# Optimization experiments

Hardware: AMD Instinct MI355X
Metric: run time of the kernel (lower is better)

The kernel has to match this reference:

```python
import jax, jax.numpy as jnp
import numpy as np

LL = 1 << 20            # Fastfood padded size (power of 2 >= DD)
DD = 1024 * 768         # out_features * in_features
OUT, IN = 1024, 768


def fwht(v):
    """Unnormalized fast Walsh-Hadamard transform over a length-2^k vector."""
    n = v.shape[0]
    h = 1
    while h < n:
        v = v.reshape(-1, 2, h)
        v = jnp.concatenate([v[:, 0] + v[:, 1], v[:, 0] - v[:, 1]], axis=-1)
        h *= 2
    return v.reshape(n)


def setup_inputs() -> dict:
    key = jax.random.key(0)
    ks = jax.random.split(key, 7)
    x = jax.random.normal(ks[0], (8, 2048, IN), dtype=jnp.float32)
    theta = jax.random.normal(ks[1], (2048,), dtype=jnp.float32)
    W_0 = jax.random.normal(ks[2], (OUT, IN), dtype=jnp.float32) * 0.02
    b = jax.random.normal(ks[3], (OUT,), dtype=jnp.float32) * 0.02
    # Rademacher +/-1 diagonal
    BB = (jax.random.bernoulli(ks[4], 0.5, (LL,)).astype(jnp.float32) * 2.0 - 1.0)
    GG = jax.random.normal(ks[5], (LL,), dtype=jnp.float32)
    Pi = jax.random.permutation(ks[6], LL).astype(jnp.int64)
    return {"x": x, "theta": theta, "W_0": W_0, "b": b, "BB": BB, "GG": GG, "Pi": Pi}


def reference(x, theta, W_0, b, BB, GG, Pi):
    # pad intrinsic parameter to LL (theta.numel() < LL branch)
    theta_pad = jnp.zeros((LL,), dtype=theta.dtype).at[: theta.shape[0]].set(theta)
    # Fastfood: H B theta -> permute -> G diag -> H
    v = fwht(BB * theta_pad)
    v = v[Pi] * GG
    v = fwht(v)
    divisor = jnp.sqrt(LL * jnp.sum(GG * GG))
    update_vec = v[:DD] / (divisor * np.sqrt(float(DD) / LL))
    W_eff = W_0 + update_vec.reshape(OUT, IN)
    return jnp.einsum("bsi,oi->bso", x, W_eff) + b
```

## Files before the change

kernel.cpp:

```cpp
#include <hip/hip_runtime.h>
#include <hip/hip_bf16.h>


#define LL (1 << 20)
#define DD (1024 * 768)
#define OUTF 1024
#define INF 768
#define MROWS 16384

typedef __attribute__((ext_vector_type(8))) short s16x8;
typedef __attribute__((ext_vector_type(4))) float f32x4;
typedef __attribute__((ext_vector_type(16))) float f32x16;

__device__ __forceinline__ unsigned short f2bf(float f) {
    union { float f; unsigned u; } v; v.f = f;
    unsigned r = v.u + 0x7FFF + ((v.u >> 16) & 1);
    return (unsigned short)(r >> 16);
}

__device__ __forceinline__ unsigned cvt_pk_bf16(float lo, float hi) {
    unsigned r;
    asm("v_cvt_pk_bf16_f32 %0, %1, %2" : "=v"(r) : "v"(lo), "v"(hi));
    return r;
}

__global__ void k0_r01(const float* __restrict__ BB, const float* __restrict__ theta,
                       float* __restrict__ r01g) {
    __shared__ float sx[2048];
    const int t = threadIdx.x;
    const int r = t >> 7, tt = t & 127, lane = t & 63;
    float v[8];
    {
        const float4 a0 = *(const float4*)&BB[r * 1024 + tt * 8];
        const float4 a1 = *(const float4*)&BB[r * 1024 + tt * 8 + 4];
        const float4 b0 = *(const float4*)&theta[r * 1024 + tt * 8];
        const float4 b1 = *(const float4*)&theta[r * 1024 + tt * 8 + 4];
        v[0] = a0.x * b0.x; v[1] = a0.y * b0.y; v[2] = a0.z * b0.z; v[3] = a0.w * b0.w;
        v[4] = a1.x * b1.x; v[5] = a1.y * b1.y; v[6] = a1.z * b1.z; v[7] = a1.w * b1.w;
    }
    float a;
    a = v[0]; v[0] = a + v[1]; v[1] = a - v[1];
    a = v[2]; v[2] = a + v[3]; v[3] = a - v[3];
    a = v[4]; v[4] = a + v[5]; v[5] = a - v[5];
    a = v[6]; v[6] = a + v[7]; v[7] = a - v[7];
    a = v[0]; v[0] = a + v[2]; v[2] = a - v[2];
    a = v[1]; v[1] = a + v[3]; v[3] = a - v[3];
    a = v[4]; v[4] = a + v[6]; v[6] = a - v[6];
    a = v[5]; v[5] = a + v[7]; v[7] = a - v[7];
    a = v[0]; v[0] = a + v[4]; v[4] = a - v[4];
    a = v[1]; v[1] = a + v[5]; v[5] = a - v[5];
    a = v[2]; v[2] = a + v[6]; v[6] = a - v[6];
    a = v[3]; v[3] = a + v[7]; v[7] = a - v[7];
    #pragma unroll
    for (int j = 0; j < 6; j++) {
        const float sgn = ((lane >> j) & 1) ? -1.0f : 1.0f;
        #pragma unroll
        for (int c = 0; c < 8; c++) {
            float o = __shfl_xor(v[c], 1 << j, 64);
            v[c] = fmaf(sgn, v[c], o);
        }
    }
    #pragma unroll
    for (int c = 0; c < 8; c++) sx[r * 1024 + tt * 8 + c] = v[c];
    __syncthreads();
    {
        const int pt = r * 1024 + (tt ^ 64) * 8;
        const float sgn = (tt & 64) ? -1.0f : 1.0f;
        #pragma unroll
        for (int c = 0; c < 8; c++) v[c] = fmaf(sgn, v[c], sx[pt + c]);
    }
    #pragma unroll
    for (int c = 0; c < 8; c++) r01g[r * 1024 + tt * 8 + c] = v[c];
}

__global__ void k1_cast(const float* __restrict__ X, ushort* __restrict__ XB) {
    const f32x4* X4 = (const f32x4*)X;
    s16x8* O = (s16x8*)XB;
    size_t i = (size_t)blockIdx.x * 256 + threadIdx.x;
    #pragma unroll
    for (int j = 0; j < 3; j++, i += 524288) {
        const f32x4 A = X4[2 * i];
        const f32x4 B = X4[2 * i + 1];
        union { s16x8 v; unsigned u[4]; } o;
        o.u[0] = cvt_pk_bf16(A.x, A.y);
        o.u[1] = cvt_pk_bf16(A.z, A.w);
        o.u[2] = cvt_pk_bf16(B.x, B.y);
        o.u[3] = cvt_pk_bf16(B.z, B.w);
        O[i] = o.v;
    }
}

__global__ __launch_bounds__(1024)
void k3_gather_fwht_lo(const int* __restrict__ Pi, const float* __restrict__ GG,
                       const float* __restrict__ r01g, f32x4* __restrict__ T2,
                       float* __restrict__ partial) {
    __shared__ float r01s[2048];
    __shared__ f32x4 sA[1024];
    __shared__ float sB[4 * 1028];
    __shared__ float ws[16];
    const int t = threadIdx.x;
    const int s_r = t >> 8, tt = t & 255, lane = t & 63;
    const int row = blockIdx.x * 4 + s_r;

    r01s[t] = r01g[t];
    r01s[t + 1024] = r01g[t + 1024];
    const int4   pv = ((const int4*)Pi)[row * 256 + tt];
    const float4 gv = ((const float4*)GG)[row * 256 + tt];
    float g2 = gv.x * gv.x + gv.y * gv.y + gv.z * gv.z + gv.w * gv.w;
    #pragma unroll
    for (int o = 32; o > 0; o >>= 1) g2 += __shfl_down(g2, o, 64);
    if (lane == 0) ws[t >> 6] = g2;
    __syncthreads();

    float v[4];
    {
        int p; float g;
        p = pv.x; g = gv.x;
        v[0] = (r01s[p & 1023] + (((p >> 10) & 1) ? -1.0f : 1.0f) * r01s[1024 + (p & 1023)]) * g;
        p = pv.y; g = gv.y;
        v[1] = (r01s[p & 1023] + (((p >> 10) & 1) ? -1.0f : 1.0f) * r01s[1024 + (p & 1023)]) * g;
        p = pv.z; g = gv.z;
        v[2] = (r01s[p & 1023] + (((p >> 10) & 1) ? -1.0f : 1.0f) * r01s[1024 + (p & 1023)]) * g;
        p = pv.w; g = gv.w;
        v[3] = (r01s[p & 1023] + (((p >> 10) & 1) ? -1.0f : 1.0f) * r01s[1024 + (p & 1023)]) * g;
    }
    float a;
    a = v[0]; v[0] = a + v[1]; v[1] = a - v[1];
    a = v[2]; v[2] = a + v[3]; v[3] = a - v[3];
    a = v[0]; v[0] = a + v[2]; v[2] = a - v[2];
    a = v[1]; v[1] = a + v[3]; v[3] = a - v[3];
    #pragma unroll
    for (int j = 0; j < 6; j++) {
        const float sgn = ((lane >> j) & 1) ? -1.0f : 1.0f;
        #pragma unroll
        for (int c = 0; c < 4; c++) {
            float o = __shfl_xor(v[c], 1 << j, 64);
            v[c] = fmaf(sgn, v[c], o);
        }
    }
    {
        f32x4 vv; vv.x = v[0]; vv.y = v[1]; vv.z = v[2]; vv.w = v[3];
        sA[t] = vv;
    }
    __syncthreads();
    {
        const int b = t & ~192;
        const f32x4 q00 = sA[b];
        const f32x4 q10 = sA[b + 64];
        const f32x4 q01 = sA[b + 128];
        const f32x4 q11 = sA[b + 192];
        const float s8 = (tt & 64) ? -1.0f : 1.0f;
        const float s9 = (tt & 128) ? -1.0f : 1.0f;
        #pragma unroll
        for (int c = 0; c < 4; c++)
            v[c] = (q00[c] + s9 * q01[c]) + s8 * (q10[c] + s9 * q11[c]);
    }
    if (t == 0) {
        float s = 0;
        #pragma unroll
        for (int i = 0; i < 16; i++) s += ws[i];
        partial[blockIdx.x] = s;
    }
    {
        f32x4 vv; vv.x = v[0]; vv.y = v[1]; vv.z = v[2]; vv.w = v[3];
        *(f32x4*)&sB[s_r * 1028 + 4 * tt] = vv;
    }
    __syncthreads();
    {
        const int rl = t & 3;
        const int lo4 = t >> 2;
        const f32x4 w = *(const f32x4*)&sB[rl * 1028 + lo4 * 4];
        T2[(size_t)lo4 * 1024 + blockIdx.x * 4 + rl] = w;
    }
}

__global__ __launch_bounds__(1024)
void k4_fwht_hi(const f32x4* __restrict__ T2, const float* __restrict__ partial,
                const float* __restrict__ W0, ushort* __restrict__ WB) {
    __shared__ f32x4 sx[1024];
    __shared__ float rw[17];
    const int t = threadIdx.x;
    const int g = blockIdx.x;
    const int lane = t & 63;

    float pr = 0.0f;
    if (t < 256) pr = partial[t];
    #pragma unroll
    for (int o = 32; o > 0; o >>= 1) pr += __shfl_down(pr, o, 64);
    if (t < 256 && lane == 0) rw[t >> 6] = pr;

    f32x4 vv = T2[(size_t)g * 1024 + t];
    #pragma unroll
    for (int j = 0; j < 6; j++) {
        const float sgn = ((lane >> j) & 1) ? -1.0f : 1.0f;
        #pragma unroll
        for (int c = 0; c < 4; c++) {
            float o = __shfl_xor(vv[c], 1 << j, 64);
            vv[c] = fmaf(sgn, vv[c], o);
        }
    }
    sx[t] = vv;
    __syncthreads();
    if (t == 0) rw[16] = rw[0] + rw[1] + rw[2] + rw[3];
    {
        const int b = t & ~192;
        const f32x4 q00 = sx[b];
        const f32x4 q10 = sx[b + 64];
        const f32x4 q01 = sx[b + 128];
        const f32x4 q11 = sx[b + 192];
        const float s6 = (t & 64) ? -1.0f : 1.0f;
        const float s7 = (t & 128) ? -1.0f : 1.0f;
        #pragma unroll
        for (int c = 0; c < 4; c++)
            vv[c] = (q00[c] + s7 * q01[c]) + s6 * (q10[c] + s7 * q11[c]);
    }
    __syncthreads();
    sx[t] = vv;
    __syncthreads();
    {
        const int b = t & ~768;
        const f32x4 q00 = sx[b];
        const f32x4 q10 = sx[b + 256];
        const f32x4 q01 = sx[b + 512];
        const f32x4 q11 = sx[b + 768];
        const float s8 = (t & 256) ? -1.0f : 1.0f;
        const float s9 = (t & 512) ? -1.0f : 1.0f;
        #pragma unroll
        for (int c = 0; c < 4; c++)
            vv[c] = (q00[c] + s9 * q01[c]) + s8 * (q10[c] + s9 * q11[c]);
    }
    if (t < 768) {
        const float scale = rsqrtf(rw[16] * (float)DD);
        const size_t d = (size_t)t * 1024 + 4 * g;
        const float4 w = *(const float4*)&W0[d];
        ushort4 o;
        o.x = f2bf(w.x + vv.x * scale);
        o.y = f2bf(w.y + vv.y * scale);
        o.z = f2bf(w.z + vv.z * scale);
        o.w = f2bf(w.w + vv.w * scale);
        *(ushort4*)&WB[d] = o;
    }
}

#define BM 128
#define BN 128
#define BK 64

__global__ __launch_bounds__(256)
void k7_gemm(const ushort* __restrict__ A, const ushort* __restrict__ B,
             const float* __restrict__ bias, float* __restrict__ C) {
    __shared__ ushort As[BM * BK];
    __shared__ ushort Bs[BN * BK];
    const int tid  = threadIdx.x;
    const int lane = tid & 63;
    const int wave = tid >> 6;
    const int m0 = blockIdx.x * BM;
    const int n0 = blockIdx.y * BN;
    const int wm = (wave & 1) * 64;
    const int wn = (wave >> 1) * 64;

    const int fr_row = lane & 31;
    const int fr_kh  = lane >> 5;

    f32x16 acc[2][2];
    #pragma unroll
    for (int i = 0; i < 2; i++)
        #pragma unroll
        for (int j = 0; j < 2; j++) acc[i][j] = (f32x16)(0.0f);

    for (int kt = 0; kt < INF; kt += BK) {
        #pragma unroll
        for (int i = 0; i < 4; i++) {
            const int s   = i * 256 + tid;
            const int row = s >> 3;
            const int kc  = (s & 7) ^ (row & 7);
            const ushort* ga = A + (size_t)(m0 + row) * INF + kt + kc * 8;
            const ushort* gb = B + (size_t)(n0 + row) * INF + kt + kc * 8;
            __builtin_amdgcn_global_load_lds(
                (const __attribute__((address_space(1))) void*)ga,
                (__attribute__((address_space(3))) void*)&As[i * 2048 + wave * 512], 16, 0, 0);
            __builtin_amdgcn_global_load_lds(
                (const __attribute__((address_space(1))) void*)gb,
                (__attribute__((address_space(3))) void*)&Bs[i * 2048 + wave * 512], 16, 0, 0);
        }
        __syncthreads();

        #pragma unroll
        for (int ks = 0; ks < 4; ks++) {
            const int kc = ks * 2 + fr_kh;
            s16x8 af[2], bf[2];
            #pragma unroll
            for (int mi = 0; mi < 2; mi++) {
                const int r = wm + mi * 32 + fr_row;
                af[mi] = *(const s16x8*)&As[(r * 8 + (kc ^ (r & 7))) * 8];
            }
            #pragma unroll
            for (int ni = 0; ni < 2; ni++) {
                const int r = wn + ni * 32 + fr_row;
                bf[ni] = *(const s16x8*)&Bs[(r * 8 + (kc ^ (r & 7))) * 8];
            }
            #pragma unroll
            for (int mi = 0; mi < 2; mi++)
                #pragma unroll
                for (int ni = 0; ni < 2; ni++)
                    acc[mi][ni] = __builtin_amdgcn_mfma_f32_32x32x16_bf16(
                        af[mi], bf[ni], acc[mi][ni], 0, 0, 0);
        }
        __syncthreads();
    }

    const int ccol = lane & 31;
    const int rbase = (lane >> 5) * 4;
    #pragma unroll
    for (int ni = 0; ni < 2; ni++) {
        const int n = n0 + wn + ni * 32 + ccol;
        const float bv = bias[n];
        #pragma unroll
        for (int mi = 0; mi < 2; mi++) {
            const int mb = m0 + wm + mi * 32 + rbase;
            #pragma unroll
            for (int r = 0; r < 16; r++) {
                const int m = mb + (r & 3) + 8 * (r >> 2);
                C[(size_t)m * OUTF + n] = acc[mi][ni][r] + bv;
            }
        }
    }
}

extern "C" void kernel_launch(void* const* d_in, const int* in_sizes, int n_in,
                              void* d_out, int out_size, void* d_ws, size_t ws_size,
                              hipStream_t stream) {
    (void)in_sizes; (void)n_in; (void)out_size; (void)ws_size;
    const float* x     = (const float*)d_in[0];
    const float* theta = (const float*)d_in[1];
    const float* W0    = (const float*)d_in[2];
    const float* bias  = (const float*)d_in[3];
    const float* BB    = (const float*)d_in[4];
    const float* GG    = (const float*)d_in[5];
    const int*   Pi    = (const int*)d_in[6];
    float* out = (float*)d_out;

    char* ws = (char*)d_ws;
    ushort* XB   = (ushort*)ws;
    f32x4*  T2   = (f32x4*)(ws + 25165824);
    ushort* WB   = (ushort*)(ws + 29360128);
    float*  R01  = (float*)(ws + 30932992);
    float*  PART = (float*)(ws + 30941184);

    k0_r01          <<<1,    256, 0, stream>>>(BB, theta, R01);
    k1_cast         <<<2048, 256, 0, stream>>>(x, XB);
    k3_gather_fwht_lo<<<256, 1024, 0, stream>>>(Pi, GG, R01, T2, PART);
    k4_fwht_hi      <<<256, 1024, 0, stream>>>(T2, PART, W0, WB);
    k7_gemm<<<dim3(MROWS/BM, OUTF/BN), 256, 0, stream>>>(XB, WB, bias, out);
}
```

Measured before the change: 170.9 us.

## Double-buffer GEMM LDS tiles and merge cast with r01 kernel

The GEMM now keeps two LDS buffers, so the global-to-LDS loads for the next K tile are issued before the MFMA work on the current tile, with the aim of overlapping memory latency with compute. The one-block r01 kernel is also folded into the x-to-bf16 cast kernel as an extra block, removing one launch. Double buffering doubles LDS use per block to 64KB, which may lower occupancy. The loop also has to keep a barrier between compute and the next overwrite of the buffer, which cannot be confirmed from the visible lines.

```diff
diff --git a/kernel.cpp b/kernel.cpp
--- a/kernel.cpp
+++ b/kernel.cpp
@@ -24,10 +24,28 @@
     return r;
 }
 
-__global__ void k0_r01(const float* __restrict__ BB, const float* __restrict__ theta,
-                       float* __restrict__ r01g) {
+__global__ void k01_cast_r01(const float* __restrict__ X, ushort* __restrict__ XB,
+                             const float* __restrict__ BB, const float* __restrict__ theta,
+                             float* __restrict__ r01g) {
     __shared__ float sx[2048];
     const int t = threadIdx.x;
+    if (blockIdx.x < 2048) {
+        const f32x4* X4 = (const f32x4*)X;
+        s16x8* O = (s16x8*)XB;
+        size_t i = (size_t)blockIdx.x * 256 + t;
+        #pragma unroll
+        for (int j = 0; j < 3; j++, i += 524288) {
+            const f32x4 A = X4[2 * i];
+            const f32x4 B = X4[2 * i + 1];
+            union { s16x8 v; unsigned u[4]; } o;
+            o.u[0] = cvt_pk_bf16(A.x, A.y);
+            o.u[1] = cvt_pk_bf16(A.z, A.w);
+            o.u[2] = cvt_pk_bf16(B.x, B.y);
+            o.u[3] = cvt_pk_bf16(B.z, B.w);
+            O[i] = o.v;
+        }
+        return;
+    }
     const int r = t >> 7, tt = t & 127, lane = t & 63;
     float v[8];
     {
@@ -73,23 +91,6 @@
     for (int c = 0; c < 8; c++) r01g[r * 1024 + tt * 8 + c] = v[c];
 }
 
-__global__ void k1_cast(const float* __restrict__ X, ushort* __restrict__ XB) {
-    const f32x4* X4 = (const f32x4*)X;
-    s16x8* O = (s16x8*)XB;
-    size_t i = (size_t)blockIdx.x * 256 + threadIdx.x;
-    #pragma unroll
-    for (int j = 0; j < 3; j++, i += 524288) {
-        const f32x4 A = X4[2 * i];
-        const f32x4 B = X4[2 * i + 1];
-        union { s16x8 v; unsigned u[4]; } o;
-        o.u[0] = cvt_pk_bf16(A.x, A.y);
-        o.u[1] = cvt_pk_bf16(A.z, A.w);
-        o.u[2] = cvt_pk_bf16(B.x, B.y);
-        o.u[3] = cvt_pk_bf16(B.z, B.w);
-        O[i] = o.v;
-    }
-}
-
 __global__ __launch_bounds__(1024)
 void k3_gather_fwht_lo(const int* __restrict__ Pi, const float* __restrict__ GG,
                        const float* __restrict__ r01g, f32x4* __restrict__ T2,
@@ -245,12 +246,13 @@
 #define BM 128
 #define BN 128
 #define BK 64
+#define KITERS (INF / BK)
 
 __global__ __launch_bounds__(256)
 void k7_gemm(const ushort* __restrict__ A, const ushort* __restrict__ B,
              const float* __restrict__ bias, float* __restrict__ C) {
-    __shared__ ushort As[BM * BK];
-    __shared__ ushort Bs[BN * BK];
+    __shared__ ushort As[2][BM * BK];
+    __shared__ ushort Bs[2][BN * BK];
     const int tid  = threadIdx.x;
     const int lane = tid & 63;
     const int wave = tid >> 6;
@@ -268,7 +270,7 @@
         #pragma unroll
         for (int j = 0; j < 2; j++) acc[i][j] = (f32x16)(0.0f);
 
-    for (int kt = 0; kt < INF; kt += BK) {
+    auto stage = [&](int bsel, int kt) {
         #pragma unroll
         for (int i = 0; i < 4; i++) {
             const int s   = i * 256 + tid;
@@ -278,13 +280,22 @@
             const ushort* gb = B + (size_t)(n0 + row) * INF + kt + kc * 8;
             __builtin_amdgcn_global_load_lds(
                 (const __attribute__((address_space(1))) void*)ga,
-                (__attribute__((address_space(3))) void*)&As[i * 2048 + wave * 512], 16, 0, 0);
+                (__attribute__((address_space(3))) void*)&As[bsel][i * 2048 + wave * 512], 16, 0, 0);
             __builtin_amdgcn_global_load_lds(
                 (const __attribute__((address_space(1))) void*)gb,
-                (__attribute__((address_space(3))) void*)&Bs[i * 2048 + wave * 512], 16, 0, 0);
-        }
-        __syncthreads();
-
+                (__attribute__((address_space(3))) void*)&Bs[bsel][i * 2048 + wave * 512], 16, 0, 0);
+        }
+    };
+
+    stage(0, 0);
+    __syncthreads();
+
+    for (int t = 0; t < KITERS; t++) {
+        const int cur = t & 1;
+        if (t + 1 < KITERS) stage(cur ^ 1, (t + 1) * BK);
+
+        const ushort* Ab = As[cur];
+        const ushort* Bb = Bs[cur];
         #pragma unroll
         for (int ks = 0; ks < 4; ks++) {
             const int kc = ks * 2 + fr_kh;
@@ -292,12 +303,12 @@
             #pragma unroll
             for (int mi = 0; mi < 2; mi++) {
                 const int r = wm + mi * 32 + fr_row;
-                af[mi] = *(const s16x8*)&As[(r * 8 + (kc ^ (r & 7))) * 8];
+                af[mi] = *(const s16x8*)&Ab[(r * 8 + (kc ^ (r & 7))) * 8];
             }
             #pragma unroll
             for (int ni = 0; ni < 2; ni++) {
                 const int r = wn + ni * 32 + fr_row;
-                bf[ni] = *(const s16x8*)&Bs[(r * 8 + (kc ^ (r & 7))) * 8];
+                bf[ni] = *(const s16x8*)&Bb[(r * 8 + (kc ^ (r & 7))) * 8];
             }
             #pragma unroll
             for (int mi = 0; mi < 2; mi++)
@@ -347,8 +358,7 @@
     float*  R01  = (float*)(ws + 30932992);
     float*  PART = (float*)(ws + 30941184);
 
-    k0_r01          <<<1,    256, 0, stream>>>(BB, theta, R01);
-    k1_cast         <<<2048, 256, 0, stream>>>(x, XB);
+    k01_cast_r01    <<<2049, 256, 0, stream>>>(x, XB, BB, theta, R01);
     k3_gather_fwht_lo<<<256, 1024, 0, stream>>>(Pi, GG, R01, T2, PART);
     k4_fwht_hi      <<<256, 1024, 0, stream>>>(T2, PART, W0, WB);
     k7_gemm<<<dim3(MROWS/BM, OUTF/BN), 256, 0, stream>>>(XB, WB, bias, out);
```

Measured after the change: 165.1 us. 1.04x faster.
